# Optimization experiments

Hardware: AMD Instinct MI355X
Metric: run time of the kernel (lower is better)

Reference implementation:

```python
import jax, jax.numpy as jnp
import numpy as np

N = 100000   # nodes
E = 1600000  # edges
H = 128      # hidden_dim
B = 4096     # number of root pairs
HOPS = 3


def setup_inputs() -> dict:
    key = jax.random.key(0)
    ks = jax.random.split(key, 12)
    s = 0.05
    return {
        "node_feat": jax.random.normal(ks[0], (N, H), jnp.float32),
        "send_embd": jax.random.normal(ks[1], (N, H), jnp.float32),
        "edge_index": jax.random.randint(ks[2], (2, E), 0, N, dtype=jnp.int32),
        "root_index": jax.random.randint(ks[3], (2 * B,), 0, N, dtype=jnp.int32),
        "agg_by_source": 1,
        "lin1_W": jax.random.normal(ks[4], (2 * H, H), jnp.float32) * s,
        "lin1_b": jnp.zeros((H,), jnp.float32),
        "gat_W": jax.random.normal(ks[5], (HOPS, H, H), jnp.float32) * s,
        "gat_asrc": jax.random.normal(ks[6], (HOPS, H), jnp.float32) * s,
        "gat_adst": jax.random.normal(ks[7], (HOPS, H), jnp.float32) * s,
        "gat_b": jnp.zeros((HOPS, H), jnp.float32),
        "lstm_Wih": jax.random.normal(ks[8], (HOPS, 2 * H, 4 * H), jnp.float32) * s,
        "lstm_Whh": jax.random.normal(ks[9], (HOPS, H, 4 * H), jnp.float32) * s,
        "lstm_b": jnp.zeros((HOPS, 4 * H), jnp.float32),
        "lin2_W": jax.random.normal(ks[10], (H, H), jnp.float32) * s,
        "lin2_b": jnp.zeros((H,), jnp.float32),
    }


def _gat_breadth(x, src, dst, W, a_src, a_dst, b):
    # GATConv(heads=1) followed by tanh (GeniePath Breadth layer)
    xw = x @ W                                  # [N, H]
    e_score = jax.nn.leaky_relu((xw @ a_src)[src] + (xw @ a_dst)[dst], 0.2)  # [E]
    # softmax over incoming edges of each destination node
    m = jax.ops.segment_max(e_score, dst, num_segments=N)
    ex = jnp.exp(e_score - m[dst])
    z = jax.ops.segment_sum(ex, dst, num_segments=N)
    alpha = ex / z[dst]                          # [E]
    agg = jax.ops.segment_sum(alpha[:, None] * xw[src], dst, num_segments=N)
    return jnp.tanh(agg + b)


def _lstm_step(inp, h, c, Wih, Whh, b):
    gates = inp @ Wih + h @ Whh + b              # [N, 4H]
    i, f, g, o = jnp.split(gates, 4, axis=-1)
    c = jax.nn.sigmoid(f) * c + jax.nn.sigmoid(i) * jnp.tanh(g)
    h = jax.nn.sigmoid(o) * jnp.tanh(c)
    return h, c


def reference(node_feat, send_embd, edge_index, root_index, agg_by_source,
              lin1_W, lin1_b, gat_W, gat_asrc, gat_adst, gat_b,
              lstm_Wih, lstm_Whh, lstm_b, lin2_W, lin2_b):
    src, dst = edge_index[0], edge_index[1]
    # Aggregation stage input: concat node embedding with broadcast embedding
    x = jnp.concatenate([node_feat, send_embd], axis=1) @ lin1_W + lin1_b  # [N, H]
    # GeniePathLazy: all breadth (GAT) layers run on the projected input x
    h_tmps = [
        _gat_breadth(x, src, dst, gat_W[i], gat_asrc[i], gat_adst[i], gat_b[i])
        for i in range(HOPS)
    ]
    # Depth: per-node LSTM over the hop axis, input = cat(h_tmp, x_prev)
    h = jnp.zeros_like(x)
    c = jnp.zeros_like(x)
    xs = x
    for i in range(HOPS):
        inp = jnp.concatenate([h_tmps[i], xs], axis=1)   # [N, 2H]
        h, c = _lstm_step(inp, h, c, lstm_Wih[i], lstm_Whh[i], lstm_b[i])
        xs = h
    out = xs @ lin2_W + lin2_b                            # [N, H]
    roots = root_index.reshape(-1, 2)
    src_nodes = roots[:, 0] if agg_by_source else roots[:, 1]
    return out[src_nodes]                                 # [B, H]
```

## Files before the change

### kernel.cpp

```cpp
#include <hip/hip_runtime.h>

constexpr int N  = 100000;
constexpr int E  = 1600000;
constexpr int H  = 128;
constexpr int NB = 4096;
constexpr int HOPS = 3;

constexpr int WOFF_L1  = 0;
constexpr int WOFF_GAT = 32768;
constexpr int WOFF_CAT = 81920;
constexpr int WOFF_L2  = 671744;
constexpr int WTOT     = 688128;

constexpr size_t ALIGN = 256;
constexpr size_t alup(size_t x) { return (x + ALIGN - 1) & ~(ALIGN - 1); }

constexpr size_t OFF_X       = 0;
constexpr size_t OFF_SSRC    = alup(OFF_X + (size_t)N * H * 4);
constexpr size_t OFF_SDST    = alup(OFF_SSRC + (size_t)3 * N * 4);
constexpr size_t OFF_WVEC    = alup(OFF_SDST + (size_t)3 * N * 4);
constexpr size_t OFF_SELMAP  = alup(OFF_WVEC + 6 * H * 4);
constexpr size_t OFF_NODELST = alup(OFF_SELMAP + (size_t)N * 4);
constexpr size_t OFF_CNT     = alup(OFF_NODELST + NB * 4);
constexpr size_t OFF_DEG     = alup(OFF_CNT + 256);
constexpr size_t OFF_OFFS    = alup(OFF_DEG + NB * 4);
constexpr size_t OFF_CURSOR  = alup(OFF_OFFS + (NB + 1) * 4);
constexpr size_t OFF_ESORT   = alup(OFF_CURSOR + NB * 4);
constexpr size_t OFF_AGGXH   = alup(OFF_ESORT + (size_t)E * 4);
constexpr size_t OFF_AGGXL   = alup(OFF_AGGXH + (size_t)3 * NB * H * 2);
constexpr size_t OFF_XSH     = alup(OFF_AGGXL + (size_t)3 * NB * H * 2);
constexpr size_t OFF_XSL     = alup(OFF_XSH + (size_t)NB * H * 2);
constexpr size_t OFF_HH      = alup(OFF_XSL + (size_t)NB * H * 2);
constexpr size_t OFF_HL      = alup(OFF_HH + (size_t)NB * H * 2);
constexpr size_t OFF_CBUF    = alup(OFF_HL + (size_t)NB * H * 2);
constexpr size_t OFF_L2OUT   = alup(OFF_CBUF + (size_t)NB * H * 4);
constexpr size_t OFF_WHI     = alup(OFF_L2OUT + (size_t)NB * H * 4);
constexpr size_t OFF_WLO     = alup(OFF_WHI + (size_t)WTOT * 2);

__device__ __forceinline__ float lrelu(float v) { return v > 0.f ? v : 0.2f * v; }
__device__ __forceinline__ float sigmoidf_(float v) { return 1.f / (1.f + __expf(-v)); }

__device__ __forceinline__ unsigned short f2bf(float f) {
  unsigned u = __float_as_uint(f);
  unsigned r = (u + 0x7FFFu + ((u >> 16) & 1u)) >> 16;
  return (unsigned short)r;
}
__device__ __forceinline__ float bf2f(unsigned short h) {
  return __uint_as_float((unsigned)h << 16);
}
__device__ __forceinline__ void split_rne(float f, unsigned short& hi, unsigned short& lo) {
  unsigned short hh = f2bf(f);
  hi = hh;
  lo = f2bf(f - bf2f(hh));
}
__device__ __forceinline__ void split_trunc(float f, short* hi, short* lo) {
  unsigned u = __float_as_uint(f);
  *hi = (short)(u >> 16);
  float r = f - __uint_as_float(u & 0xFFFF0000u);
  *lo = (short)(__float_as_uint(r) >> 16);
}

typedef short bf16x8 __attribute__((ext_vector_type(8)));
typedef float f32x4  __attribute__((ext_vector_type(4)));

#define MFMA3(ACC, AH, AL, BH, BL)                                               \
  ACC = __builtin_amdgcn_mfma_f32_16x16x32_bf16(AH, BH, ACC, 0, 0, 0);           \
  ACC = __builtin_amdgcn_mfma_f32_16x16x32_bf16(AH, BL, ACC, 0, 0, 0);           \
  ACC = __builtin_amdgcn_mfma_f32_16x16x32_bf16(AL, BH, ACC, 0, 0, 0);

__global__ void init_ws(int* __restrict__ sel_map, int* __restrict__ deg,
                        int* __restrict__ cursor, int* __restrict__ cnt,
                        float* __restrict__ cbuf, unsigned short* __restrict__ hh,
                        unsigned short* __restrict__ hl, int* __restrict__ need_flag) {
  int i = blockIdx.x * 256 + threadIdx.x;
  int stride = gridDim.x * 256;
  for (int n = i; n < N; n += stride) { sel_map[n] = -1; need_flag[n] = 0; }
  for (int n = i; n < NB; n += stride) { deg[n] = 0; cursor[n] = 0; }
  if (i < 64) cnt[i] = 0;
  for (int n = i; n < NB * H; n += stride) { cbuf[n] = 0.f; hh[n] = 0; hl[n] = 0; }
}

__global__ void prep_kernel(const float* __restrict__ gat_W,
                            const float* __restrict__ a_src,
                            const float* __restrict__ a_dst,
                            float* __restrict__ wvec,
                            const float* __restrict__ lin1_W,
                            const float* __restrict__ Wih,
                            const float* __restrict__ Whh,
                            const float* __restrict__ lin2_W,
                            unsigned short* __restrict__ whi,
                            unsigned short* __restrict__ wlo) {
  if (blockIdx.x < 6) {
    int i = blockIdx.x >> 1, which = blockIdx.x & 1;
    int k = threadIdx.x;
    __shared__ float av[H];
    if (k < H) av[k] = which ? a_dst[i * H + k] : a_src[i * H + k];
    __syncthreads();
    if (k >= H) return;
    const float* Wr = gat_W + (size_t)i * H * H + (size_t)k * H;
    float s = 0.f;
    #pragma unroll 8
    for (int j = 0; j < H; j++) s = fmaf(Wr[j], av[j], s);
    wvec[(i * 2 + which) * H + k] = s;
    return;
  }
  int idx = (blockIdx.x - 6) * 256 + threadIdx.x;
  if (idx >= WTOT) return;
  float v;
  if (idx < WOFF_GAT) {
    int rel = idx;
    int e = rel & 7, lane = (rel >> 3) & 63, tile = rel >> 9;
    int nl = lane & 15, quad = lane >> 4;
    int c = tile & 7, t = tile >> 3;
    int n = c * 16 + nl, k = t * 32 + quad * 8 + e;
    v = lin1_W[k * 128 + n];
  } else if (idx < WOFF_CAT) {
    int rel = idx - WOFF_GAT;
    int hop = rel / 16384; rel %= 16384;
    int e = rel & 7, lane = (rel >> 3) & 63, tile = rel >> 9;
    int nl = lane & 15, quad = lane >> 4;
    int c = tile & 7, t = tile >> 3;
    int n = c * 16 + nl, k = t * 32 + quad * 8 + e;
    v = gat_W[hop * 16384 + k * 128 + n];
  } else if (idx < WOFF_L2) {
    int rel = idx - WOFF_CAT;
    int hop = rel / 196608; rel %= 196608;
    int e = rel & 7, lane = (rel >> 3) & 63, tile = rel >> 9;
    int nl = lane & 15, quad = lane >> 4;
    int c = tile & 31, t = tile >> 5;
    int ftile = c >> 2, g = c & 3;
    int col = g * 128 + ftile * 16 + nl;
    int k = t * 32 + quad * 8 + e;
    v = (k < 256) ? Wih[hop * 131072 + k * 512 + col]
                  : Whh[hop * 65536 + (k - 256) * 512 + col];
  } else {
    int rel = idx - WOFF_L2;
    int e = rel & 7, lane = (rel >> 3) & 63, tile = rel >> 9;
    int nl = lane & 15, quad = lane >> 4;
    int c = tile & 7, t = tile >> 3;
    int n = c * 16 + nl, k = t * 32 + quad * 8 + e;
    v = lin2_W[k * 128 + n];
  }
  unsigned short hh, ll;
  split_rne(v, hh, ll);
  whi[idx] = hh;
  wlo[idx] = ll;
}

__global__ void roots_assign(const int* __restrict__ root, const int* __restrict__ aggp,
                             int* __restrict__ sel_map, int* __restrict__ node_list,
                             int* __restrict__ cnt, int* __restrict__ need_flag) {
  int b = blockIdx.x * 256 + threadIdx.x;
  if (b >= NB) return;
  int node = root[2 * b + (aggp[0] ? 0 : 1)];
  need_flag[node] = 1;
  int old = atomicCAS(&sel_map[node], -1, -2);
  if (old == -1) {
    int c = atomicAdd(cnt, 1);
    sel_map[node] = c;
    node_list[c] = node;
  }
}

__global__ __launch_bounds__(256)
void gemm_lin1(const float* __restrict__ a0, const float* __restrict__ a1,
               const unsigned short* __restrict__ Bth,
               const unsigned short* __restrict__ Btl,
               const float* __restrict__ bias, float* __restrict__ Cc,
               const float* __restrict__ wvec,
               float* __restrict__ s_src, float* __restrict__ s_dst,
               const int* __restrict__ need_list, const int* __restrict__ need_cnt) {
  const int t = threadIdx.x, lane = t & 63, wave = t >> 6;
  const int nl = lane & 15, quad = lane >> 4;
  const int nneed = need_cnt[0];
  if (blockIdx.x * 128 >= nneed) return;
  const int rt = blockIdx.x * 128 + wave * 32;

  int rowi[2];
  #pragma unroll
  for (int i = 0; i < 2; i++) {
    int gr = rt + i * 16 + nl;
    rowi[i] = (gr < nneed) ? need_list[gr] : -1;
  }

  f32x4 acc[2][8];
  #pragma unroll
  for (int i = 0; i < 2; i++)
    #pragma unroll
    for (int c = 0; c < 8; c++) acc[i][c] = (f32x4){0.f, 0.f, 0.f, 0.f};

  #pragma unroll
  for (int kt = 0; kt < 8; kt++) {
    const float* A = (kt < 4) ? a0 : a1;
    const int kk = (kt & 3) * 32 + quad * 8;
    bf16x8 ahi[2], alo[2];
    #pragma unroll
    for (int i = 0; i < 2; i++) {
      int row = rowi[i];
      float4 v0 = make_float4(0.f, 0.f, 0.f, 0.f), v1 = v0;
      if (row >= 0) {
        const float* p = A + (size_t)row * H + kk;
        v0 = *(const float4*)p;
        v1 = *(const float4*)(p + 4);
      }
      float af[8] = {v0.x, v0.y, v0.z, v0.w, v1.x, v1.y, v1.z, v1.w};
      #pragma unroll
      for (int j = 0; j < 8; j++) {
        short h_, l_;
        split_trunc(af[j], &h_, &l_);
        ahi[i][j] = h_;
        alo[i][j] = l_;
      }
    }
    #pragma unroll
    for (int c = 0; c < 8; c++) {
      size_t boff = ((size_t)(kt * 8 + c) * 64 + lane) * 8;
      bf16x8 bh = *(const bf16x8*)(Bth + boff);
      bf16x8 bl = *(const bf16x8*)(Btl + boff);
      #pragma unroll
      for (int i = 0; i < 2; i++) { MFMA3(acc[i][c], ahi[i], alo[i], bh, bl); }
    }
  }

  float bv[8], wvf[6][8];
  #pragma unroll
  for (int c = 0; c < 8; c++) {
    int col = c * 16 + nl;
    bv[c] = bias[col];
    #pragma unroll
    for (int v6 = 0; v6 < 6; v6++) wvf[v6][c] = wvec[v6 * 128 + col];
  }
  #pragma unroll
  for (int i = 0; i < 2; i++)
    #pragma unroll
    for (int r = 0; r < 4; r++) {
      int gr = rt + i * 16 + quad * 4 + r;
      if (gr >= nneed) continue;
      int row = need_list[gr];
      float* cr = Cc + (size_t)row * H;
      float sc[6] = {0.f, 0.f, 0.f, 0.f, 0.f, 0.f};
      #pragma unroll
      for (int c = 0; c < 8; c++) {
        float val = acc[i][c][r] + bv[c];
        cr[c * 16 + nl] = val;
        #pragma unroll
        for (int v6 = 0; v6 < 6; v6++) sc[v6] = fmaf(val, wvf[v6][c], sc[v6]);
      }
      #pragma unroll
      for (int m = 1; m < 16; m <<= 1)
        #pragma unroll
        for (int v6 = 0; v6 < 6; v6++) sc[v6] += __shfl_xor(sc[v6], m);
      if (nl == 0) {
        #pragma unroll
        for (int h3 = 0; h3 < 3; h3++) {
          s_src[h3 * N + row] = sc[2 * h3 + 0];
          s_dst[h3 * N + row] = sc[2 * h3 + 1];
        }
      }
    }
}

__global__ void count_edges(const int* __restrict__ ei, const int* __restrict__ sel_map,
                            int* __restrict__ deg) {
  int e = blockIdx.x * 256 + threadIdx.x;
  if (e >= E) return;
  int d = sel_map[ei[E + e]];
  if (d >= 0) atomicAdd(&deg[d], 1);
}

__global__ __launch_bounds__(1024)
void scan_kernel(const int* __restrict__ deg, int* __restrict__ offs) {
  __shared__ int part[1024];
  int t = threadIdx.x;
  int base = t * 4;
  int v0 = deg[base], v1 = deg[base + 1], v2 = deg[base + 2], v3 = deg[base + 3];
  int s = v0 + v1 + v2 + v3;
  part[t] = s;
  __syncthreads();
  for (int off = 1; off < 1024; off <<= 1) {
    int tmp = (t >= off) ? part[t - off] : 0;
    __syncthreads();
    part[t] += tmp;
    __syncthreads();
  }
  int run = part[t] - s;
  offs[base] = run; run += v0;
  offs[base + 1] = run; run += v1;
  offs[base + 2] = run; run += v2;
  offs[base + 3] = run;
  if (t == 1023) offs[NB] = part[1023];
}

__global__ void scatter_edges2(const int* __restrict__ ei, const int* __restrict__ sel_map,
                               const int* __restrict__ offs, int* __restrict__ cursor,
                               int* __restrict__ es_sorted, int* __restrict__ need_flag) {
  int e = blockIdx.x * 256 + threadIdx.x;
  if (e >= E) return;
  int d = sel_map[ei[E + e]];
  if (d >= 0) {
    int p = atomicAdd(&cursor[d], 1);
    int s = ei[e];
    es_sorted[offs[d] + p] = s;
    need_flag[s] = 1;
  }
}

__global__ void compact_need(const int* __restrict__ need_flag,
                             int* __restrict__ need_list, int* __restrict__ need_cnt) {
  int i = blockIdx.x * 256 + threadIdx.x;
  bool f = (i < N) && (need_flag[i] != 0);
  unsigned long long mask = __ballot(f);
  int lane = threadIdx.x & 63;
  int wcnt = __popcll(mask);
  int base = 0;
  if (lane == 0 && wcnt > 0) base = atomicAdd(need_cnt, wcnt);
  base = __shfl(base, 0);
  if (f) {
    int prefix = __popcll(mask & ((1ull << lane) - 1ull));
    need_list[base + prefix] = i;
  }
}

__global__ __launch_bounds__(128)
void gat_node_kernel(const int* __restrict__ node_list, const int* __restrict__ cntp,
                     const int* __restrict__ offs, const int* __restrict__ es_sorted,
                     const float* __restrict__ x, const float* __restrict__ s_src,
                     const float* __restrict__ s_dst,
                     unsigned short* __restrict__ aggxh, unsigned short* __restrict__ aggxl,
                     unsigned short* __restrict__ xsh, unsigned short* __restrict__ xsl) {
  int c = blockIdx.x;
  if (c >= cntp[0]) return;
  int t = threadIdx.x;
  int n = node_list[c];
  {
    float xv = x[(size_t)n * H + t];
    unsigned short vh, vl;
    split_rne(xv, vh, vl);
    xsh[(size_t)c * H + t] = vh;
    xsl[(size_t)c * H + t] = vl;
  }
  float sd0 = s_dst[0 * N + n], sd1 = s_dst[1 * N + n], sd2 = s_dst[2 * N + n];
  int e0 = offs[c], e1 = offs[c + 1];
  float m0 = -1e30f, m1 = -1e30f, m2 = -1e30f;
  for (int e = e0 + t; e < e1; e += 128) {
    int s = es_sorted[e];
    m0 = fmaxf(m0, lrelu(s_src[0 * N + s] + sd0));
    m1 = fmaxf(m1, lrelu(s_src[1 * N + s] + sd1));
    m2 = fmaxf(m2, lrelu(s_src[2 * N + s] + sd2));
  }
  __shared__ float red[3][128];
  red[0][t] = m0; red[1][t] = m1; red[2][t] = m2;
  __syncthreads();
  for (int s2 = 64; s2 > 0; s2 >>= 1) {
    if (t < s2) {
      red[0][t] = fmaxf(red[0][t], red[0][t + s2]);
      red[1][t] = fmaxf(red[1][t], red[1][t + s2]);
      red[2][t] = fmaxf(red[2][t], red[2][t + s2]);
    }
    __syncthreads();
  }
  m0 = red[0][0]; m1 = red[1][0]; m2 = red[2][0];
  float u0 = 0.f, u1 = 0.f, u2 = 0.f, z0 = 0.f, z1 = 0.f, z2 = 0.f;
  for (int e = e0; e < e1; e++) {
    int s = es_sorted[e];
    float xs = x[(size_t)s * H + t];
    float ex0 = __expf(lrelu(s_src[0 * N + s] + sd0) - m0);
    float ex1 = __expf(lrelu(s_src[1 * N + s] + sd1) - m1);
    float ex2 = __expf(lrelu(s_src[2 * N + s] + sd2) - m2);
    z0 += ex0; z1 += ex1; z2 += ex2;
    u0 = fmaf(ex0, xs, u0); u1 = fmaf(ex1, xs, u1); u2 = fmaf(ex2, xs, u2);
  }
  size_t cb = (size_t)c * H + t;
  bool any = e1 > e0;
  float v0 = any ? u0 / z0 : 0.f;
  float v1 = any ? u1 / z1 : 0.f;
  float v2 = any ? u2 / z2 : 0.f;
  unsigned short vh, vl;
  split_rne(v0, vh, vl); aggxh[0 * ((size_t)NB * H) + cb] = vh; aggxl[0 * ((size_t)NB * H) + cb] = vl;
  split_rne(v1, vh, vl); aggxh[1 * ((size_t)NB * H) + cb] = vh; aggxl[1 * ((size_t)NB * H) + cb] = vl;
  split_rne(v2, vh, vl); aggxh[2 * ((size_t)NB * H) + cb] = vh; aggxl[2 * ((size_t)NB * H) + cb] = vl;
}

__global__ __launch_bounds__(256)
void hop_fused(const unsigned short* __restrict__ agh, const unsigned short* __restrict__ agl,
               const unsigned short* __restrict__ gWh, const unsigned short* __restrict__ gWl,
               const float* __restrict__ gbias,
               const unsigned short* __restrict__ x1h, const unsigned short* __restrict__ x1l,
               const unsigned short* __restrict__ CWh, const unsigned short* __restrict__ CWl,
               const float* __restrict__ lbias,
               float* __restrict__ cbuf, unsigned short* __restrict__ hh,
               unsigned short* __restrict__ hl,
               const unsigned short* __restrict__ L2h, const unsigned short* __restrict__ L2l,
               const float* __restrict__ lin2_b, float* __restrict__ l2out, int do_lin2) {
  __shared__ unsigned short Hh[16 * 136];
  __shared__ unsigned short Hl[16 * 136];
  const int t = threadIdx.x, lane = t & 63, wave = t >> 6;
  const int nl = lane & 15, quad = lane >> 4;
  const int r0 = blockIdx.x * 16;

  f32x4 acc1[2];
  #pragma unroll
  for (int j = 0; j < 2; j++) acc1[j] = (f32x4){0.f, 0.f, 0.f, 0.f};
  #pragma unroll
  for (int kt = 0; kt < 4; kt++) {
    size_t aoff = (size_t)(r0 + nl) * H + kt * 32 + quad * 8;
    bf16x8 ah = *(const bf16x8*)(agh + aoff);
    bf16x8 al = *(const bf16x8*)(agl + aoff);
    #pragma unroll
    for (int j = 0; j < 2; j++) {
      size_t boff = ((size_t)(kt * 8 + 2 * wave + j) * 64 + lane) * 8;
      bf16x8 bh = *(const bf16x8*)(gWh + boff);
      bf16x8 bl = *(const bf16x8*)(gWl + boff);
      MFMA3(acc1[j], ah, al, bh, bl);
    }
  }
  #pragma unroll
  for (int j = 0; j < 2; j++) {
    int col = wave * 32 + j * 16 + nl;
    float bv = gbias[col];
    #pragma unroll
    for (int r = 0; r < 4; r++) {
      int rl = quad * 4 + r;
      float v = tanhf(acc1[j][r] + bv);
      unsigned short vh, vl2;
      split_rne(v, vh, vl2);
      Hh[rl * 136 + col] = vh;
      Hl[rl * 136 + col] = vl2;
    }
  }
  __syncthreads();

  f32x4 acc2[8];
  #pragma unroll
  for (int j = 0; j < 8; j++) acc2[j] = (f32x4){0.f, 0.f, 0.f, 0.f};
  for (int kt = 0; kt < 12; kt++) {
    int kk = (kt & 3) * 32 + quad * 8;
    bf16x8 ah, al;
    if (kt < 4) {
      ah = *(const bf16x8*)&Hh[nl * 136 + kk];
      al = *(const bf16x8*)&Hl[nl * 136 + kk];
    } else {
      const unsigned short* ph = (kt < 8) ? x1h : hh;
      const unsigned short* pl = (kt < 8) ? x1l : hl;
      size_t aoff = (size_t)(r0 + nl) * H + kk;
      ah = *(const bf16x8*)(ph + aoff);
      al = *(const bf16x8*)(pl + aoff);
    }
    #pragma unroll
    for (int cc = 0; cc < 8; cc++) {
      size_t boff = ((size_t)(kt * 32 + 8 * wave + cc) * 64 + lane) * 8;
      bf16x8 bh = *(const bf16x8*)(CWh + boff);
      bf16x8 bl = *(const bf16x8*)(CWl + boff);
      MFMA3(acc2[cc], ah, al, bh, bl);
    }
  }
  __syncthreads();

  #pragma unroll
  for (int ft = 0; ft < 2; ft++) {
    int f = (2 * wave + ft) * 16 + nl;
    float b_i = lbias[0 * 128 + f], b_f = lbias[1 * 128 + f];
    float b_g = lbias[2 * 128 + f], b_o = lbias[3 * 128 + f];
    #pragma unroll
    for (int r = 0; r < 4; r++) {
      int rl = quad * 4 + r;
      size_t id = (size_t)(r0 + rl) * H + f;
      float gi = acc2[ft * 4 + 0][r] + b_i;
      float gf = acc2[ft * 4 + 1][r] + b_f;
      float gg = acc2[ft * 4 + 2][r] + b_g;
      float go = acc2[ft * 4 + 3][r] + b_o;
      float cp = cbuf[id];
      float cn = sigmoidf_(gf) * cp + sigmoidf_(gi) * tanhf(gg);
      float hn = sigmoidf_(go) * tanhf(cn);
      cbuf[id] = cn;
      unsigned short vh, vl2;
      split_rne(hn, vh, vl2);
      hh[id] = vh;
      hl[id] = vl2;
      if (do_lin2) { Hh[rl * 136 + f] = vh; Hl[rl * 136 + f] = vl2; }
    }
  }

  if (!do_lin2) return;
  __syncthreads();
  f32x4 acc3[2];
  #pragma unroll
  for (int j = 0; j < 2; j++) acc3[j] = (f32x4){0.f, 0.f, 0.f, 0.f};
  #pragma unroll
  for (int kt = 0; kt < 4; kt++) {
    int kk = kt * 32 + quad * 8;
    bf16x8 ah = *(const bf16x8*)&Hh[nl * 136 + kk];
    bf16x8 al = *(const bf16x8*)&Hl[nl * 136 + kk];
    #pragma unroll
    for (int j = 0; j < 2; j++) {
      size_t boff = ((size_t)(kt * 8 + 2 * wave + j) * 64 + lane) * 8;
      bf16x8 bh = *(const bf16x8*)(L2h + boff);
      bf16x8 bl = *(const bf16x8*)(L2l + boff);
      MFMA3(acc3[j], ah, al, bh, bl);
    }
  }
  #pragma unroll
  for (int j = 0; j < 2; j++) {
    int col = wave * 32 + j * 16 + nl;
    float bv = lin2_b[col];
    #pragma unroll
    for (int r = 0; r < 4; r++) {
      int row = r0 + quad * 4 + r;
      l2out[(size_t)row * H + col] = acc3[j][r] + bv;
    }
  }
}

__global__ void scatter_out(const float* __restrict__ l2out, const int* __restrict__ sel_map,
                            const int* __restrict__ root, const int* __restrict__ aggp,
                            float* __restrict__ out) {
  int id = blockIdx.x * 256 + threadIdx.x;
  if (id >= NB * H) return;
  int b = id >> 7, f = id & 127;
  int node = root[2 * b + (aggp[0] ? 0 : 1)];
  int c = sel_map[node];
  out[id] = l2out[(size_t)c * H + f];
}

extern "C" void kernel_launch(void* const* d_in, const int* in_sizes, int n_in,
                              void* d_out, int out_size, void* d_ws, size_t ws_size,
                              hipStream_t stream) {
  const float* node_feat = (const float*)d_in[0];
  const float* send_embd = (const float*)d_in[1];
  const int*   edge_idx  = (const int*)d_in[2];
  const int*   root_idx  = (const int*)d_in[3];
  const int*   aggp      = (const int*)d_in[4];
  const float* lin1_W    = (const float*)d_in[5];
  const float* lin1_b    = (const float*)d_in[6];
  const float* gat_W     = (const float*)d_in[7];
  const float* gat_asrc  = (const float*)d_in[8];
  const float* gat_adst  = (const float*)d_in[9];
  const float* gat_b     = (const float*)d_in[10];
  const float* lstm_Wih  = (const float*)d_in[11];
  const float* lstm_Whh  = (const float*)d_in[12];
  const float* lstm_b    = (const float*)d_in[13];
  const float* lin2_W    = (const float*)d_in[14];
  const float* lin2_b    = (const float*)d_in[15];
  float* out = (float*)d_out;

  char* ws = (char*)d_ws;
  float* x       = (float*)(ws + OFF_X);
  float* s_src   = (float*)(ws + OFF_SSRC);
  float* s_dst   = (float*)(ws + OFF_SDST);
  float* wvec    = (float*)(ws + OFF_WVEC);
  int*   sel_map = (int*)(ws + OFF_SELMAP);
  int*   nodelst = (int*)(ws + OFF_NODELST);
  int*   cnt     = (int*)(ws + OFF_CNT);
  int*   deg     = (int*)(ws + OFF_DEG);
  int*   offs    = (int*)(ws + OFF_OFFS);
  int*   cursor  = (int*)(ws + OFF_CURSOR);
  int*   esort   = (int*)(ws + OFF_ESORT);
  unsigned short* aggxh = (unsigned short*)(ws + OFF_AGGXH);
  unsigned short* aggxl = (unsigned short*)(ws + OFF_AGGXL);
  unsigned short* xsh   = (unsigned short*)(ws + OFF_XSH);
  unsigned short* xsl   = (unsigned short*)(ws + OFF_XSL);
  unsigned short* hh    = (unsigned short*)(ws + OFF_HH);
  unsigned short* hl    = (unsigned short*)(ws + OFF_HL);
  float* cbuf    = (float*)(ws + OFF_CBUF);
  float* l2out   = (float*)(ws + OFF_L2OUT);
  unsigned short* whi = (unsigned short*)(ws + OFF_WHI);
  unsigned short* wlo = (unsigned short*)(ws + OFF_WLO);

  int* need_flag = (int*)(ws + OFF_AGGXH);
  int* need_list = need_flag + N;
  int* need_cnt  = cnt + 1;

  init_ws<<<2048, 256, 0, stream>>>(sel_map, deg, cursor, cnt, cbuf, hh, hl, need_flag);
  prep_kernel<<<6 + (WTOT + 255) / 256, 256, 0, stream>>>(
      gat_W, gat_asrc, gat_adst, wvec, lin1_W, lstm_Wih, lstm_Whh, lin2_W, whi, wlo);
  roots_assign<<<(NB + 255) / 256, 256, 0, stream>>>(root_idx, aggp, sel_map, nodelst, cnt,
                                                     need_flag);

  count_edges<<<(E + 255) / 256, 256, 0, stream>>>(edge_idx, sel_map, deg);
  scan_kernel<<<1, 1024, 0, stream>>>(deg, offs);
  scatter_edges2<<<(E + 255) / 256, 256, 0, stream>>>(edge_idx, sel_map, offs, cursor, esort,
                                                      need_flag);
  compact_need<<<(N + 255) / 256, 256, 0, stream>>>(need_flag, need_list, need_cnt);

  gemm_lin1<<<(N + 127) / 128, 256, 0, stream>>>(
      node_feat, send_embd, whi + WOFF_L1, wlo + WOFF_L1, lin1_b, x,
      wvec, s_src, s_dst, need_list, need_cnt);

  gat_node_kernel<<<NB, 128, 0, stream>>>(nodelst, cnt, offs, esort, x, s_src, s_dst,
                                          aggxh, aggxl, xsh, xsl);

  for (int i = 0; i < HOPS; i++) {
    const unsigned short* x1h = (i == 0) ? xsh : hh;
    const unsigned short* x1l = (i == 0) ? xsl : hl;
    hop_fused<<<NB / 16, 256, 0, stream>>>(
        aggxh + (size_t)i * NB * H, aggxl + (size_t)i * NB * H,
        whi + WOFF_GAT + i * 16384, wlo + WOFF_GAT + i * 16384,
        gat_b + (size_t)i * H,
        x1h, x1l,
        whi + WOFF_CAT + i * 196608, wlo + WOFF_CAT + i * 196608,
        lstm_b + (size_t)i * 512,
        cbuf, hh, hl,
        whi + WOFF_L2, wlo + WOFF_L2, lin2_b, l2out,
        (i == HOPS - 1) ? 1 : 0);
  }

  scatter_out<<<(NB * H + 255) / 256, 256, 0, stream>>>(l2out, sel_map, root_idx, aggp, out);
}
```

Measured before the change: 366.0 us.

## Compact selected edges in first pass and prefetch lin1 A rows

The edge counting pass now also writes a packed (dst,src) list of the edges whose destination is a root, using wave ballots and block-level atomics. The scatter pass then walks only this compact list instead of re-reading all 1.6M edges and their sel_map lookups. Separately, gemm_lin1 loads all of its A-row float4s up front before the MFMA loop to expose memory-level parallelism, with launch bounds raised to 2 blocks per CU. The packing assumes src < 2^17 and reuses the x buffer region for the list before x is written; the prefetch raises register pressure.

```diff
diff --git a/kernel.cpp b/kernel.cpp
--- a/kernel.cpp
+++ b/kernel.cpp
@@ -162,7 +162,85 @@
   }
 }
 
-__global__ __launch_bounds__(256)
+__global__ void edge_pass1(const int* __restrict__ ei, const int* __restrict__ sel_map,
+                           int* __restrict__ deg, int* __restrict__ plist,
+                           int* __restrict__ plist_cnt) {
+  __shared__ int lcnt;
+  __shared__ int lbase;
+  __shared__ int wbase[4];
+  const int tid = threadIdx.x, lane = tid & 63, wave = tid >> 6;
+  if (tid == 0) lcnt = 0;
+  __syncthreads();
+  int e = blockIdx.x * 256 + tid;
+  int d = -1, s = 0;
+  if (e < E) {
+    d = sel_map[ei[E + e]];
+    if (d >= 0) { s = ei[e]; atomicAdd(&deg[d], 1); }
+  }
+  bool f = d >= 0;
+  unsigned long long mask = __ballot(f);
+  int wpre = __popcll(mask & ((1ull << lane) - 1ull));
+  int wcnt = __popcll(mask);
+  if (lane == 0) wbase[wave] = atomicAdd(&lcnt, wcnt);
+  __syncthreads();
+  if (tid == 0) lbase = (lcnt > 0) ? atomicAdd(plist_cnt, lcnt) : 0;
+  __syncthreads();
+  if (f) plist[lbase + wbase[wave] + wpre] = (d << 17) | s;
+}
+
+__global__ __launch_bounds__(1024)
+void scan_kernel(const int* __restrict__ deg, int* __restrict__ offs) {
+  __shared__ int part[1024];
+  int t = threadIdx.x;
+  int base = t * 4;
+  int v0 = deg[base], v1 = deg[base + 1], v2 = deg[base + 2], v3 = deg[base + 3];
+  int s = v0 + v1 + v2 + v3;
+  part[t] = s;
+  __syncthreads();
+  for (int off = 1; off < 1024; off <<= 1) {
+    int tmp = (t >= off) ? part[t - off] : 0;
+    __syncthreads();
+    part[t] += tmp;
+    __syncthreads();
+  }
+  int run = part[t] - s;
+  offs[base] = run; run += v0;
+  offs[base + 1] = run; run += v1;
+  offs[base + 2] = run; run += v2;
+  offs[base + 3] = run;
+  if (t == 1023) offs[NB] = part[1023];
+}
+
+__global__ void edge_pass2(const int* __restrict__ plist, const int* __restrict__ plist_cnt,
+                           const int* __restrict__ offs, int* __restrict__ cursor,
+                           int* __restrict__ es_sorted, int* __restrict__ need_flag) {
+  int np = plist_cnt[0];
+  for (int i = blockIdx.x * 256 + threadIdx.x; i < np; i += gridDim.x * 256) {
+    int pk = plist[i];
+    int d = pk >> 17, s = pk & 0x1FFFF;
+    int p = atomicAdd(&cursor[d], 1);
+    es_sorted[offs[d] + p] = s;
+    need_flag[s] = 1;
+  }
+}
+
+__global__ void compact_need(const int* __restrict__ need_flag,
+                             int* __restrict__ need_list, int* __restrict__ need_cnt) {
+  int i = blockIdx.x * 256 + threadIdx.x;
+  bool f = (i < N) && (need_flag[i] != 0);
+  unsigned long long mask = __ballot(f);
+  int lane = threadIdx.x & 63;
+  int wcnt = __popcll(mask);
+  int base = 0;
+  if (lane == 0 && wcnt > 0) base = atomicAdd(need_cnt, wcnt);
+  base = __shfl(base, 0);
+  if (f) {
+    int prefix = __popcll(mask & ((1ull << lane) - 1ull));
+    need_list[base + prefix] = i;
+  }
+}
+
+__global__ __launch_bounds__(256, 2)
 void gemm_lin1(const float* __restrict__ a0, const float* __restrict__ a1,
                const unsigned short* __restrict__ Bth,
                const unsigned short* __restrict__ Btl,
@@ -183,26 +261,36 @@
     rowi[i] = (gr < nneed) ? need_list[gr] : -1;
   }
 
-  f32x4 acc[2][8];
-  #pragma unroll
-  for (int i = 0; i < 2; i++)
-    #pragma unroll
-    for (int c = 0; c < 8; c++) acc[i][c] = (f32x4){0.f, 0.f, 0.f, 0.f};
-
+  float4 va[2][8][2];
   #pragma unroll
   for (int kt = 0; kt < 8; kt++) {
     const float* A = (kt < 4) ? a0 : a1;
     const int kk = (kt & 3) * 32 + quad * 8;
-    bf16x8 ahi[2], alo[2];
     #pragma unroll
     for (int i = 0; i < 2; i++) {
-      int row = rowi[i];
       float4 v0 = make_float4(0.f, 0.f, 0.f, 0.f), v1 = v0;
-      if (row >= 0) {
-        const float* p = A + (size_t)row * H + kk;
+      if (rowi[i] >= 0) {
+        const float* p = A + (size_t)rowi[i] * H + kk;
         v0 = *(const float4*)p;
         v1 = *(const float4*)(p + 4);
       }
+      va[i][kt][0] = v0;
+      va[i][kt][1] = v1;
+    }
+  }
+
+  f32x4 acc[2][8];
+  #pragma unroll
+  for (int i = 0; i < 2; i++)
+    #pragma unroll
+    for (int c = 0; c < 8; c++) acc[i][c] = (f32x4){0.f, 0.f, 0.f, 0.f};
+
+  #pragma unroll
+  for (int kt = 0; kt < 8; kt++) {
+    bf16x8 ahi[2], alo[2];
+    #pragma unroll
+    for (int i = 0; i < 2; i++) {
+      float4 v0 = va[i][kt][0], v1 = va[i][kt][1];
       float af[8] = {v0.x, v0.y, v0.z, v0.w, v1.x, v1.y, v1.z, v1.w};
       #pragma unroll
       for (int j = 0; j < 8; j++) {
@@ -260,67 +348,6 @@
     }
 }
 
-__global__ void count_edges(const int* __restrict__ ei, const int* __restrict__ sel_map,
-                            int* __restrict__ deg) {
-  int e = blockIdx.x * 256 + threadIdx.x;
-  if (e >= E) return;
-  int d = sel_map[ei[E + e]];
-  if (d >= 0) atomicAdd(&deg[d], 1);
-}
-
-__global__ __launch_bounds__(1024)
-void scan_kernel(const int* __restrict__ deg, int* __restrict__ offs) {
-  __shared__ int part[1024];
-  int t = threadIdx.x;
-  int base = t * 4;
-  int v0 = deg[base], v1 = deg[base + 1], v2 = deg[base + 2], v3 = deg[base + 3];
-  int s = v0 + v1 + v2 + v3;
-  part[t] = s;
-  __syncthreads();
-  for (int off = 1; off < 1024; off <<= 1) {
-    int tmp = (t >= off) ? part[t - off] : 0;
-    __syncthreads();
-    part[t] += tmp;
-    __syncthreads();
-  }
-  int run = part[t] - s;
-  offs[base] = run; run += v0;
-  offs[base + 1] = run; run += v1;
-  offs[base + 2] = run; run += v2;
-  offs[base + 3] = run;
-  if (t == 1023) offs[NB] = part[1023];
-}
-
-__global__ void scatter_edges2(const int* __restrict__ ei, const int* __restrict__ sel_map,
-                               const int* __restrict__ offs, int* __restrict__ cursor,
-                               int* __restrict__ es_sorted, int* __restrict__ need_flag) {
-  int e = blockIdx.x * 256 + threadIdx.x;
-  if (e >= E) return;
-  int d = sel_map[ei[E + e]];
-  if (d >= 0) {
-    int p = atomicAdd(&cursor[d], 1);
-    int s = ei[e];
-    es_sorted[offs[d] + p] = s;
-    need_flag[s] = 1;
-  }
-}
-
-__global__ void compact_need(const int* __restrict__ need_flag,
-                             int* __restrict__ need_list, int* __restrict__ need_cnt) {
-  int i = blockIdx.x * 256 + threadIdx.x;
-  bool f = (i < N) && (need_flag[i] != 0);
-  unsigned long long mask = __ballot(f);
-  int lane = threadIdx.x & 63;
-  int wcnt = __popcll(mask);
-  int base = 0;
-  if (lane == 0 && wcnt > 0) base = atomicAdd(need_cnt, wcnt);
-  base = __shfl(base, 0);
-  if (f) {
-    int prefix = __popcll(mask & ((1ull << lane) - 1ull));
-    need_list[base + prefix] = i;
-  }
-}
-
 __global__ __launch_bounds__(128)
 void gat_node_kernel(const int* __restrict__ node_list, const int* __restrict__ cntp,
                      const int* __restrict__ offs, const int* __restrict__ es_sorted,
@@ -569,6 +596,8 @@
   int* need_flag = (int*)(ws + OFF_AGGXH);
   int* need_list = need_flag + N;
   int* need_cnt  = cnt + 1;
+  int* plist     = (int*)(ws + OFF_X);
+  int* plist_cnt = cnt + 2;
 
   init_ws<<<2048, 256, 0, stream>>>(sel_map, deg, cursor, cnt, cbuf, hh, hl, need_flag);
   prep_kernel<<<6 + (WTOT + 255) / 256, 256, 0, stream>>>(
@@ -576,10 +605,9 @@
   roots_assign<<<(NB + 255) / 256, 256, 0, stream>>>(root_idx, aggp, sel_map, nodelst, cnt,
                                                      need_flag);
 
-  count_edges<<<(E + 255) / 256, 256, 0, stream>>>(edge_idx, sel_map, deg);
+  edge_pass1<<<(E + 255) / 256, 256, 0, stream>>>(edge_idx, sel_map, deg, plist, plist_cnt);
   scan_kernel<<<1, 1024, 0, stream>>>(deg, offs);
-  scatter_edges2<<<(E + 255) / 256, 256, 0, stream>>>(edge_idx, sel_map, offs, cursor, esort,
-                                                      need_flag);
+  edge_pass2<<<1024, 256, 0, stream>>>(plist, plist_cnt, offs, cursor, esort, need_flag);
   compact_need<<<(N + 255) / 256, 256, 0, stream>>>(need_flag, need_list, need_cnt);
 
   gemm_lin1<<<(N + 127) / 128, 256, 0, stream>>>(
```

Measured after the change: 421.5 us. 15.2% more time.
